# Performance work log

Hardware: AMD Instinct MI355X
Metric: run time of the kernel (lower is better)

The kernel has to match this reference:

```python
import jax, jax.numpy as jnp
import numpy as np

N_NODES = 50000
N_EDGES = 1600000
F_IN = 128
HID = 128
N_CLS = 16


def setup_inputs() -> dict:
    key = jax.random.key(0)
    ks = jax.random.split(key, 8)
    x = jax.random.normal(ks[0], (N_NODES, F_IN), dtype=jnp.float32)
    edge_index = jax.random.randint(ks[1], (2, N_EDGES), 0, N_NODES, dtype=jnp.int64)
    W1 = jax.random.normal(ks[2], (F_IN, HID), dtype=jnp.float32) * (1.0 / np.sqrt(F_IN))
    b1 = jnp.zeros((HID,), dtype=jnp.float32)
    W2 = jax.random.normal(ks[3], (HID, HID), dtype=jnp.float32) * (1.0 / np.sqrt(HID))
    b2 = jnp.zeros((HID,), dtype=jnp.float32)
    W3 = jax.random.normal(ks[4], (HID, N_CLS), dtype=jnp.float32) * (1.0 / np.sqrt(HID))
    b3 = jnp.zeros((N_CLS,), dtype=jnp.float32)
    return {"x": x, "edge_index": edge_index, "W1": W1, "b1": b1,
            "W2": W2, "b2": b2, "W3": W3, "b3": b3}


def _gcn_norm(edge_index, n_nodes, dtype):
    # PyG gcn_norm with add_self_loops=True, improved=False
    loops = jnp.arange(n_nodes, dtype=edge_index.dtype)
    row = jnp.concatenate([edge_index[0], loops])  # source j
    col = jnp.concatenate([edge_index[1], loops])  # target i
    deg = jax.ops.segment_sum(jnp.ones(row.shape[0], dtype=dtype), col,
                              num_segments=n_nodes)
    dinv = jnp.where(deg > 0, jax.lax.rsqrt(deg), 0.0)
    norm = dinv[row] * dinv[col]  # [E + N]
    return row, col, norm


def _gcn_conv(h, W, b, row, col, norm, n_nodes):
    h = h @ W                              # [N, out] linear first (PyG order)
    msg = h[row] * norm[:, None]           # gather + per-edge scale
    agg = jax.ops.segment_sum(msg, col, num_segments=n_nodes)  # scatter-add
    return agg + b


def reference(x, edge_index, W1, b1, W2, b2, W3, b3):
    n = x.shape[0]
    row, col, norm = _gcn_norm(edge_index, n, x.dtype)
    h = jax.nn.relu(_gcn_conv(x, W1, b1, row, col, norm, n))
    h = jax.nn.relu(_gcn_conv(h, W2, b2, row, col, norm, n))
    h = jax.nn.relu(_gcn_conv(h, W3, b3, row, col, norm, n))
    return h
```

## Files before the change

### kernel.cpp

```cpp
#include <hip/hip_runtime.h>
#include <hip/hip_fp16.h>


static inline int cdiv(int a, int b) { return (a + b - 1) / b; }

__global__ __launch_bounds__(256) void k_zero_int(int* p, int n) {
    int i = blockIdx.x * 256 + threadIdx.x;
    if (i < n) p[i] = 0;
}

__global__ __launch_bounds__(256) void k_count(const int* __restrict__ col, int* cnt, int e) {
    int i = blockIdx.x * 256 + threadIdx.x;
    if (i < e) atomicAdd(&cnt[col[i]], 1);
}

__global__ __launch_bounds__(256) void k_scanA(const int* __restrict__ cnt, int* bsum,
                                               float* __restrict__ dinv, int n) {
    __shared__ int s[256];
    int t = threadIdx.x;
    int i = blockIdx.x * 256 + t;
    int v = (i < n) ? cnt[i] : 0;
    if (i < n) dinv[i] = rsqrtf((float)(v + 1));
    s[t] = v;
    __syncthreads();
    for (int off = 128; off > 0; off >>= 1) {
        if (t < off) s[t] += s[t + off];
        __syncthreads();
    }
    if (t == 0) bsum[blockIdx.x] = s[0];
}

__global__ __launch_bounds__(256) void k_scanB(int* bsum, int nb) {
    __shared__ int s[256];
    int t = threadIdx.x;
    int v = (t < nb) ? bsum[t] : 0;
    s[t] = v;
    for (int off = 1; off < 256; off <<= 1) {
        __syncthreads();
        int x = (t >= off) ? s[t - off] : 0;
        __syncthreads();
        s[t] += x;
    }
    __syncthreads();
    if (t < nb) bsum[t] = s[t] - v;
}

__global__ __launch_bounds__(256) void k_scanC(const int* __restrict__ cnt, const int* __restrict__ bsum,
                                               int* offs, int* cur, int n) {
    __shared__ int s[256];
    int t = threadIdx.x;
    int i = blockIdx.x * 256 + t;
    int v = (i < n) ? cnt[i] : 0;
    s[t] = v;
    for (int off = 1; off < 256; off <<= 1) {
        __syncthreads();
        int x = (t >= off) ? s[t - off] : 0;
        __syncthreads();
        s[t] += x;
    }
    __syncthreads();
    int ov = bsum[blockIdx.x] + s[t] - v;
    if (i <= n) offs[i] = ov;
    if (i < n) cur[i] = ov;
}

__global__ __launch_bounds__(256) void k_fill_xcd(const int* __restrict__ row, const int* __restrict__ col,
                                                  int* cur, unsigned short* __restrict__ csr,
                                                  int e, int n, int nblk) {
    int g = blockIdx.x & 7;
    int b = blockIdx.x >> 3;
    int rs = (n + 7) >> 3;
    int lo = g * rs;
    int hi = min(lo + rs, n);
    int stride = nblk * 256;
    for (int i = b * 256 + threadIdx.x; i < e; i += stride) {
        int c = col[i];
        if (c >= lo && c < hi) {
            int pos = atomicAdd(&cur[c], 1);
            csr[pos] = (unsigned short)row[i];
        }
    }
}

__global__ __launch_bounds__(256) void k_gemm128(const float* __restrict__ X, const float* __restrict__ W,
                                                 const float* __restrict__ dinv,
                                                 __half* __restrict__ Ah, int n) {
    __shared__ float sW[128 * 128];
    __shared__ float sX[16][128];
    int tid = threadIdx.x;
    for (int i = tid; i < 4096; i += 256)
        ((float4*)sW)[i] = ((const float4*)W)[i];

    int row0 = blockIdx.x * 128;
    int tx = tid & 15, ty = tid >> 4;
    float acc[8][8];
    #pragma unroll
    for (int i = 0; i < 8; ++i)
        #pragma unroll
        for (int j = 0; j < 8; ++j) acc[i][j] = 0.f;

    for (int k0 = 0; k0 < 128; k0 += 16) {
        __syncthreads();
        #pragma unroll
        for (int i = tid; i < 512; i += 256) {
            int r = i >> 2, kq = i & 3;
            int gr = row0 + r;
            float4 v = (gr < n) ? ((const float4*)X)[(size_t)gr * 32 + (k0 >> 2) + kq]
                                : make_float4(0.f, 0.f, 0.f, 0.f);
            sX[kq * 4 + 0][r] = v.x;
            sX[kq * 4 + 1][r] = v.y;
            sX[kq * 4 + 2][r] = v.z;
            sX[kq * 4 + 3][r] = v.w;
        }
        __syncthreads();
        #pragma unroll
        for (int kk = 0; kk < 16; ++kk) {
            float a[8], b[8];
            *(float4*)&a[0] = *(const float4*)&sX[kk][ty * 8];
            *(float4*)&a[4] = *(const float4*)&sX[kk][ty * 8 + 4];
            *(float4*)&b[0] = *(const float4*)&sW[(k0 + kk) * 128 + tx * 8];
            *(float4*)&b[4] = *(const float4*)&sW[(k0 + kk) * 128 + tx * 8 + 4];
            #pragma unroll
            for (int i = 0; i < 8; ++i)
                #pragma unroll
                for (int j = 0; j < 8; ++j)
                    acc[i][j] = fmaf(a[i], b[j], acc[i][j]);
        }
    }
    #pragma unroll
    for (int i = 0; i < 8; ++i) {
        int gr = row0 + ty * 8 + i;
        if (gr < n) {
            float di = dinv[gr];
            union { uint4 u; __half2 h[4]; } pk;
            pk.h[0] = __floats2half2_rn(di * acc[i][0], di * acc[i][1]);
            pk.h[1] = __floats2half2_rn(di * acc[i][2], di * acc[i][3]);
            pk.h[2] = __floats2half2_rn(di * acc[i][4], di * acc[i][5]);
            pk.h[3] = __floats2half2_rn(di * acc[i][6], di * acc[i][7]);
            ((uint4*)Ah)[(size_t)gr * 16 + tx] = pk.u;
        }
    }
}

__global__ __launch_bounds__(256) void k_gemm16(const float* __restrict__ X, const float* __restrict__ W,
                                                const float* __restrict__ dinv,
                                                __half* __restrict__ Ch, int n) {
    __shared__ float sX[16 * 132];
    __shared__ float sW[128 * 16];
    int tid = threadIdx.x;
    for (int i = tid; i < 512; i += 256)
        ((float4*)sW)[i] = ((const float4*)W)[i];
    int row0 = blockIdx.x * 16;
    for (int i = tid; i < 512; i += 256) {
        int r = i >> 5, c = i & 31;
        int gr = row0 + r;
        float4 v = (gr < n) ? ((const float4*)X)[(size_t)gr * 32 + c]
                            : make_float4(0.f, 0.f, 0.f, 0.f);
        *(float4*)&sX[r * 132 + c * 4] = v;
    }
    __syncthreads();

    int rl = tid >> 4, cj = tid & 15;
    float acc = 0.f;
    #pragma unroll 8
    for (int k = 0; k < 128; ++k)
        acc = fmaf(sX[rl * 132 + k], sW[k * 16 + cj], acc);
    int gr = row0 + rl;
    if (gr < n) Ch[(size_t)gr * 16 + cj] = __float2half_rn(dinv[gr] * acc);
}

__global__ __launch_bounds__(256) void k_agg128(const __half* __restrict__ Hh, const unsigned short* __restrict__ csr,
                                                const int* __restrict__ offs, const float* __restrict__ dinv,
                                                const float* __restrict__ b, float* __restrict__ out, int n) {
    int node = (blockIdx.x * 256 + threadIdx.x) >> 6;
    if (node >= n) return;
    int lane = threadIdx.x & 63;
    int sub  = lane & 31;
    int half = lane >> 5;
    const uint2* H2 = (const uint2*)Hh;
    int ed = offs[node], end = offs[node + 1];
    float4 acc = make_float4(0.f, 0.f, 0.f, 0.f);

    #define EDGE_ADD(R)                                                          \
        {                                                                        \
            uint2 q = H2[(size_t)(R) * 32 + sub];                                \
            float2 f01 = __half22float2(*(const __half2*)&q.x);                  \
            float2 f23 = __half22float2(*(const __half2*)&q.y);                  \
            acc.x += f01.x; acc.y += f01.y;                                      \
            acc.z += f23.x; acc.w += f23.y;                                      \
        }

    for (; ed + 7 < end; ed += 8) {
        int r0 = csr[ed     + half];
        int r1 = csr[ed + 2 + half];
        int r2 = csr[ed + 4 + half];
        int r3 = csr[ed + 6 + half];
        EDGE_ADD(r0); EDGE_ADD(r1); EDGE_ADD(r2); EDGE_ADD(r3);
    }
    #pragma unroll
    for (int s = 0; s < 4; ++s) {
        int idx = ed + 2 * s + half;
        if (idx < end) {
            int r = csr[idx];
            EDGE_ADD(r);
        }
    }
    #undef EDGE_ADD

    acc.x += __shfl_xor(acc.x, 32);
    acc.y += __shfl_xor(acc.y, 32);
    acc.z += __shfl_xor(acc.z, 32);
    acc.w += __shfl_xor(acc.w, 32);

    float di = dinv[node];
    uint2 qh = H2[(size_t)node * 32 + sub];
    float2 h01 = __half22float2(*(const __half2*)&qh.x);
    float2 h23 = __half22float2(*(const __half2*)&qh.y);
    float4 bv = ((const float4*)b)[sub];
    float4 o;
    o.x = fmaxf(fmaf(di, acc.x + h01.x, bv.x), 0.f);
    o.y = fmaxf(fmaf(di, acc.y + h01.y, bv.y), 0.f);
    o.z = fmaxf(fmaf(di, acc.z + h23.x, bv.z), 0.f);
    o.w = fmaxf(fmaf(di, acc.w + h23.y, bv.w), 0.f);
    if (half == 0)
        ((float4*)out)[(size_t)node * 32 + sub] = o;
}

__global__ __launch_bounds__(256) void k_agg16(const __half* __restrict__ Ch, const unsigned short* __restrict__ csr,
                                               const int* __restrict__ offs, const float* __restrict__ dinv,
                                               const float* __restrict__ b, float* __restrict__ out, int n) {
    int t = blockIdx.x * 256 + threadIdx.x;
    int node = t >> 3;
    if (node >= n) return;
    int lane = t & 7;
    int sub  = lane & 3;
    int half = lane >> 2;
    const uint2* C2 = (const uint2*)Ch;
    int ed = offs[node], end = offs[node + 1];
    float4 acc = make_float4(0.f, 0.f, 0.f, 0.f);

    #define EDGE_ADD16(R)                                                        \
        {                                                                        \
            uint2 q = C2[(size_t)(R) * 4 + sub];                                 \
            float2 f01 = __half22float2(*(const __half2*)&q.x);                  \
            float2 f23 = __half22float2(*(const __half2*)&q.y);                  \
            acc.x += f01.x; acc.y += f01.y;                                      \
            acc.z += f23.x; acc.w += f23.y;                                      \
        }

    for (; ed + 3 < end; ed += 4) {
        int r0 = csr[ed     + half];
        int r1 = csr[ed + 2 + half];
        EDGE_ADD16(r0); EDGE_ADD16(r1);
    }
    #pragma unroll
    for (int s = 0; s < 2; ++s) {
        int idx = ed + 2 * s + half;
        if (idx < end) {
            int r = csr[idx];
            EDGE_ADD16(r);
        }
    }
    #undef EDGE_ADD16

    acc.x += __shfl_xor(acc.x, 4);
    acc.y += __shfl_xor(acc.y, 4);
    acc.z += __shfl_xor(acc.z, 4);
    acc.w += __shfl_xor(acc.w, 4);

    float di = dinv[node];
    uint2 qh = C2[(size_t)node * 4 + sub];
    float2 h01 = __half22float2(*(const __half2*)&qh.x);
    float2 h23 = __half22float2(*(const __half2*)&qh.y);
    float4 bv = ((const float4*)b)[sub];
    float4 o;
    o.x = fmaxf(fmaf(di, acc.x + h01.x, bv.x), 0.f);
    o.y = fmaxf(fmaf(di, acc.y + h01.y, bv.y), 0.f);
    o.z = fmaxf(fmaf(di, acc.z + h23.x, bv.z), 0.f);
    o.w = fmaxf(fmaf(di, acc.w + h23.y, bv.w), 0.f);
    if (half == 0)
        ((float4*)out)[(size_t)node * 4 + sub] = o;
}

extern "C" void kernel_launch(void* const* d_in, const int* in_sizes, int n_in,
                              void* d_out, int out_size, void* d_ws, size_t ws_size,
                              hipStream_t stream) {
    const float* x  = (const float*)d_in[0];
    const int*   ei = (const int*)d_in[1];
    const float* W1 = (const float*)d_in[2];
    const float* b1 = (const float*)d_in[3];
    const float* W2 = (const float*)d_in[4];
    const float* b2 = (const float*)d_in[5];
    const float* W3 = (const float*)d_in[6];
    const float* b3 = (const float*)d_in[7];

    const int n = in_sizes[0] / 128;
    const int e = in_sizes[1] / 2;
    const int* row = ei;
    const int* col = ei + e;

    unsigned short* csr = (unsigned short*)d_ws;
    __half* Ah  = (__half*)(csr + ((e + 1) & ~1));
    float*  B   = (float*)(Ah + (size_t)n * 128);
    __half* Ch  = (__half*)(B + (size_t)n * 128);
    float* dinv = (float*)(Ch + (size_t)n * 16);
    int*   offs = (int*)(dinv + n);
    int*   cnt  = offs + (n + 1);
    int*   cur  = cnt + n;
    int*   bsum = cur + n;
    float* out  = (float*)d_out;

    const int nb = cdiv(n + 1, 256);
    const int fillBlocks = 256;

    k_zero_int<<<cdiv(n, 256), 256, 0, stream>>>(cnt, n);
    k_count   <<<cdiv(e, 256), 256, 0, stream>>>(col, cnt, e);
    k_scanA   <<<nb, 256, 0, stream>>>(cnt, bsum, dinv, n);
    k_scanB   <<<1, 256, 0, stream>>>(bsum, nb);
    k_scanC   <<<nb, 256, 0, stream>>>(cnt, bsum, offs, cur, n);
    k_fill_xcd<<<8 * fillBlocks, 256, 0, stream>>>(row, col, cur, csr, e, n, fillBlocks);

    k_gemm128<<<cdiv(n, 128), 256, 0, stream>>>(x, W1, dinv, Ah, n);
    k_agg128 <<<cdiv(n * 64, 256), 256, 0, stream>>>(Ah, csr, offs, dinv, b1, B, n);
    k_gemm128<<<cdiv(n, 128), 256, 0, stream>>>(B, W2, dinv, Ah, n);
    k_agg128 <<<cdiv(n * 64, 256), 256, 0, stream>>>(Ah, csr, offs, dinv, b2, B, n);
    k_gemm16 <<<cdiv(n, 16), 256, 0, stream>>>(B, W3, dinv, Ch, n);
    k_agg16  <<<cdiv(n * 8, 256), 256, 0, stream>>>(Ch, csr, offs, dinv, b3, out, n);
}
```

Before: 365.1 us.

## Pre-bin edges by destination XCD group before CSR fill

```diff
diff --git a/kernel.cpp b/kernel.cpp
--- a/kernel.cpp
+++ b/kernel.cpp
@@ -4,14 +4,43 @@
 
 static inline int cdiv(int a, int b) { return (a + b - 1) / b; }
 
-__global__ __launch_bounds__(256) void k_zero_int(int* p, int n) {
+__global__ __launch_bounds__(256) void k_zero_init(int* cnt, int n, int* gcur, int cap) {
     int i = blockIdx.x * 256 + threadIdx.x;
-    if (i < n) p[i] = 0;
-}
-
-__global__ __launch_bounds__(256) void k_count(const int* __restrict__ col, int* cnt, int e) {
-    int i = blockIdx.x * 256 + threadIdx.x;
-    if (i < e) atomicAdd(&cnt[col[i]], 1);
+    if (i < n) cnt[i] = 0;
+    if (i < 64) gcur[i] = i * cap;
+}
+
+__global__ __launch_bounds__(256) void k_binA(const int* __restrict__ row, const int* __restrict__ col,
+                                              int* cnt, int* gcur, unsigned int* __restrict__ tmp,
+                                              int e, int rs, int nblk) {
+    int sc = blockIdx.x & 7;
+    int lane = threadIdx.x & 63;
+    int stride = nblk * 256;
+    for (int base_i = blockIdx.x * 256; base_i < e; base_i += stride) {
+        int i = base_i + threadIdx.x;
+        bool valid = i < e;
+        int c = 0, r = 0, g = -1;
+        if (valid) {
+            c = col[i];
+            r = row[i];
+            atomicAdd(&cnt[c], 1);
+            g = c / rs;
+        }
+        #pragma unroll
+        for (int g8 = 0; g8 < 8; ++g8) {
+            unsigned long long m = __ballot(valid && (g == g8));
+            if (m == 0ull) continue;
+            int n8 = __popcll(m);
+            int leader = __ffsll((unsigned long long)m) - 1;
+            int base = 0;
+            if (lane == leader) base = atomicAdd(&gcur[g8 * 8 + sc], n8);
+            base = __shfl(base, leader);
+            if (valid && (g == g8)) {
+                int rank = __popcll(m & ((1ull << lane) - 1ull));
+                tmp[base + rank] = ((unsigned int)(c - g8 * rs) << 16) | (unsigned int)r;
+            }
+        }
+    }
 }
 
 __global__ __launch_bounds__(256) void k_scanA(const int* __restrict__ cnt, int* bsum,
@@ -64,20 +93,23 @@
     if (i < n) cur[i] = ov;
 }
 
-__global__ __launch_bounds__(256) void k_fill_xcd(const int* __restrict__ row, const int* __restrict__ col,
-                                                  int* cur, unsigned short* __restrict__ csr,
-                                                  int e, int n, int nblk) {
+__global__ __launch_bounds__(256) void k_fillB(const unsigned int* __restrict__ tmp,
+                                               const int* __restrict__ gcur, int* cur,
+                                               unsigned short* __restrict__ csr,
+                                               int rs, int cap, int nblk) {
     int g = blockIdx.x & 7;
     int b = blockIdx.x >> 3;
-    int rs = (n + 7) >> 3;
-    int lo = g * rs;
-    int hi = min(lo + rs, n);
+    int base_c = g * rs;
     int stride = nblk * 256;
-    for (int i = b * 256 + threadIdx.x; i < e; i += stride) {
-        int c = col[i];
-        if (c >= lo && c < hi) {
+    for (int s = 0; s < 8; ++s) {
+        int rid = g * 8 + s;
+        int rbase = rid * cap;
+        int rend = gcur[rid];
+        for (int i = rbase + b * 256 + threadIdx.x; i < rend; i += stride) {
+            unsigned int u = tmp[i];
+            int c = base_c + (int)(u >> 16);
             int pos = atomicAdd(&cur[c], 1);
-            csr[pos] = (unsigned short)row[i];
+            csr[pos] = (unsigned short)(u & 0xffffu);
         }
     }
 }
@@ -298,9 +330,12 @@
     const int e = in_sizes[1] / 2;
     const int* row = ei;
     const int* col = ei + e;
+    const int rs  = (n + 7) >> 3;
+    const int cap = e / 64 + 8192;
 
     unsigned short* csr = (unsigned short*)d_ws;
-    __half* Ah  = (__half*)(csr + ((e + 1) & ~1));
+    unsigned int*   tmp = (unsigned int*)(csr + ((e + 1) & ~1));
+    __half* Ah  = (__half*)(tmp + (size_t)64 * cap);
     float*  B   = (float*)(Ah + (size_t)n * 128);
     __half* Ch  = (__half*)(B + (size_t)n * 128);
     float* dinv = (float*)(Ch + (size_t)n * 16);
@@ -308,17 +343,19 @@
     int*   cnt  = offs + (n + 1);
     int*   cur  = cnt + n;
     int*   bsum = cur + n;
+    int*   gcur = bsum + 256;
     float* out  = (float*)d_out;
 
     const int nb = cdiv(n + 1, 256);
-    const int fillBlocks = 256;
-
-    k_zero_int<<<cdiv(n, 256), 256, 0, stream>>>(cnt, n);
-    k_count   <<<cdiv(e, 256), 256, 0, stream>>>(col, cnt, e);
-    k_scanA   <<<nb, 256, 0, stream>>>(cnt, bsum, dinv, n);
-    k_scanB   <<<1, 256, 0, stream>>>(bsum, nb);
-    k_scanC   <<<nb, 256, 0, stream>>>(cnt, bsum, offs, cur, n);
-    k_fill_xcd<<<8 * fillBlocks, 256, 0, stream>>>(row, col, cur, csr, e, n, fillBlocks);
+    const int binBlocks   = 1024;
+    const int fillBBlocks = 128;
+
+    k_zero_init<<<cdiv(n, 256), 256, 0, stream>>>(cnt, n, gcur, cap);
+    k_binA     <<<binBlocks, 256, 0, stream>>>(row, col, cnt, gcur, tmp, e, rs, binBlocks);
+    k_scanA    <<<nb, 256, 0, stream>>>(cnt, bsum, dinv, n);
+    k_scanB    <<<1, 256, 0, stream>>>(bsum, nb);
+    k_scanC    <<<nb, 256, 0, stream>>>(cnt, bsum, offs, cur, n);
+    k_fillB    <<<8 * fillBBlocks, 256, 0, stream>>>(tmp, gcur, cur, csr, rs, cap, fillBBlocks);
 
     k_gemm128<<<cdiv(n, 128), 256, 0, stream>>>(x, W1, dinv, Ah, n);
     k_agg128 <<<cdiv(n * 64, 256), 256, 0, stream>>>(Ah, csr, offs, dinv, b1, B, n);
```

Result: slower. 1.432 ms (+292.2%).
